# Performance work log

Measured on AMD Instinct MI355X. Metric: run time of the kernel, lower is better.

## Reference

```python
import jax, jax.numpy as jnp
import numpy as np

B, S, F, D, H, L, FF, M, NH, D2, O = 4, 1024, 20, 512, 8, 4, 2048, 32, 3, 256, 1
HD = D // H


def ln(x, g, b, eps=1e-5):
    m = jnp.mean(x, -1, keepdims=True)
    v = jnp.mean((x - m) ** 2, -1, keepdims=True)
    return (x - m) / jnp.sqrt(v + eps) * g + b


def posenc(seq_len, d_model):
    pos = jnp.arange(seq_len, dtype=jnp.float32)[:, None]
    div = jnp.exp(jnp.arange(0, d_model, 2, dtype=jnp.float32) * (-np.log(10000.0) / d_model))
    pe = jnp.zeros((seq_len, d_model), jnp.float32)
    pe = pe.at[:, 0::2].set(jnp.sin(pos * div)).at[:, 1::2].set(jnp.cos(pos * div))
    return pe


def setup_inputs():
    key = jax.random.key(0)
    ks = iter(jax.random.split(key, 64))
    g = lambda shape, s=0.02: jax.random.normal(next(ks), shape, jnp.float32) * s
    z = lambda shape: jnp.zeros(shape, jnp.float32)
    o = lambda shape: jnp.ones(shape, jnp.float32)
    return {
        'x': jax.random.normal(next(ks), (B, S, F), jnp.float32),
        'in_W': g((F, D)), 'in_b': z((D,)), 'in_ln_g': o((D,)), 'in_ln_b': z((D,)),
        'ln1_g': o((L, D)), 'ln1_b': z((L, D)),
        'Wq': g((L, D, D)), 'bq': z((L, D)), 'Wk': g((L, D, D)), 'bk': z((L, D)),
        'Wv': g((L, D, D)), 'bv': z((L, D)), 'Wo': g((L, D, D)), 'bo': z((L, D)),
        'rel': g((L, 2 * M + 1, HD)),
        'ln2_g': o((L, D)), 'ln2_b': z((L, D)),
        'W1': g((L, D, FF)), 'b1': z((L, FF)), 'W2': g((L, FF, D)), 'b2': z((L, D)),
        'gWq': g((D, D)), 'gbq': z((D,)), 'gWk': g((D, D)), 'gbk': z((D,)),
        'gWv': g((D, D)), 'gbv': z((D,)), 'gWo': g((D, D)), 'gbo': z((D,)),
        'hW1': g((NH, D, D2)), 'hb1': z((NH, D2)), 'hln_g': o((NH, D2)), 'hln_b': z((NH, D2)),
        'hW2': g((NH, D2, O)), 'hb2': z((NH, O)),
    }


def _heads(xx, Wq, bq, Wk, bk, Wv, bv):
    # project and split into heads -> [B,H,S,HD]
    q = (xx @ Wq + bq).reshape(B, S, H, HD).transpose(0, 2, 1, 3)
    k = (xx @ Wk + bk).reshape(B, S, H, HD).transpose(0, 2, 1, 3)
    v = (xx @ Wv + bv).reshape(B, S, H, HD).transpose(0, 2, 1, 3)
    return q, k, v


def _block(x, l1g, l1b, Wq, bq, Wk, bk, Wv, bv, Wo, bo, rel, l2g, l2b, W1, b1, W2, b2):
    xn = ln(x, l1g, l1b)
    q, k, v = _heads(xn, Wq, bq, Wk, bk, Wv, bv)
    scores = jnp.einsum('bhqd,bhkd->bhqk', q, k) / jnp.sqrt(jnp.float32(HD))
    pos = jnp.arange(S)
    rel_idx = jnp.clip(pos[None, :] - pos[:, None], -M, M) + M  # [S,S]
    rel_enc = rel[rel_idx]  # [S,S,HD]
    # relative-position bias (NOT scaled by sqrt(HD), matching the torch code)
    scores = scores + jnp.einsum('bhqd,qkd->bhqk', q, rel_enc)
    w = jax.nn.softmax(scores, axis=-1)
    out = jnp.einsum('bhqk,bhkd->bhqd', w, v).transpose(0, 2, 1, 3).reshape(B, S, D)
    x = x + out @ Wo + bo
    xn = ln(x, l2g, l2b)
    ff = jax.nn.gelu(xn @ W1 + b1, approximate=False) @ W2 + b2
    return x + ff


def _forward(x, in_W, in_b, in_ln_g, in_ln_b, ln1_g, ln1_b, Wq, bq, Wk, bk, Wv, bv, Wo, bo, rel,
             ln2_g, ln2_b, W1, b1, W2, b2, gWq, gbq, gWk, gbk, gWv, gbv, gWo, gbo,
             hW1, hb1, hln_g, hln_b, hW2, hb2):
    h = ln(x @ in_W + in_b, in_ln_g, in_ln_b)
    h = h + posenc(S, D)[None]
    for l in range(L):
        h = _block(h, ln1_g[l], ln1_b[l], Wq[l], bq[l], Wk[l], bk[l], Wv[l], bv[l],
                   Wo[l], bo[l], rel[l], ln2_g[l], ln2_b[l], W1[l], b1[l], W2[l], b2[l])
    # global multi-head self-attention (standard scaled dot-product)
    q, k, v = _heads(h, gWq, gbq, gWk, gbk, gWv, gbv)
    w = jax.nn.softmax(jnp.einsum('bhqd,bhkd->bhqk', q, k) / jnp.sqrt(jnp.float32(HD)), axis=-1)
    go = jnp.einsum('bhqk,bhkd->bhqd', w, v).transpose(0, 2, 1, 3).reshape(B, S, D) @ gWo + gbo
    ctx = go[:, -1, :]  # last-timestep context [B,D]
    y = jnp.einsum('bd,hde->bhe', ctx, hW1) + hb1  # [B,NH,D2]
    y = jax.nn.relu(ln(y, hln_g, hln_b))
    return jnp.einsum('bhe,heo->bho', y, hW2) + hb2  # [B,NH,O]


def reference(x, in_W, in_b, in_ln_g, in_ln_b, ln1_g, ln1_b, Wq, bq, Wk, bk, Wv, bv, Wo, bo, rel,
              ln2_g, ln2_b, W1, b1, W2, b2, gWq, gbq, gWk, gbk, gWv, gbv, gWo, gbo,
              hW1, hb1, hln_g, hln_b, hW2, hb2):
    return _forward(x, in_W, in_b, in_ln_g, in_ln_b, ln1_g, ln1_b, Wq, bq, Wk, bk, Wv, bv, Wo, bo,
                    rel, ln2_g, ln2_b, W1, b1, W2, b2, gWq, gbq, gWk, gbk, gWv, gbv, gWo, gbo,
                    hW1, hb1, hln_g, hln_b, hW2, hb2)
```

## Files before the change

kernel.cpp:

```cpp
#include <hip/hip_runtime.h>
#include <math.h>

#define DEV __device__ __forceinline__

constexpr int BSD = 4 * 1024 * 512;

typedef __attribute__((ext_vector_type(8))) short bf16x8;
typedef __attribute__((ext_vector_type(4))) float f32x4;

typedef __attribute__((address_space(1))) const void global_cvoid;
typedef __attribute__((address_space(3))) void lds_void;

DEV ushort f2b(float f) {
  union { float f; uint u; } x{f};
  uint r = x.u + 0x7fff + ((x.u >> 16) & 1);
  return (ushort)(r >> 16);
}
DEV float b2f(ushort u) {
  union { uint u; float f; } x{(uint)u << 16};
  return x.f;
}
DEV int swz128(int b) { return b ^ (((b >> 7) & 7) << 4); }

DEV float wave_sum(float v) {
#pragma unroll
  for (int m = 32; m >= 1; m >>= 1) v += __shfl_xor(v, m, 64);
  return v;
}
DEV float wave_max(float v) {
#pragma unroll
  for (int m = 32; m >= 1; m >>= 1) v = fmaxf(v, __shfl_xor(v, m, 64));
  return v;
}
DEV float block_sum(float v, float* sm) {
  v = wave_sum(v);
  __syncthreads();
  if ((threadIdx.x & 63) == 0) sm[threadIdx.x >> 6] = v;
  __syncthreads();
  return sm[0] + sm[1] + sm[2] + sm[3];
}
DEV float block_max(float v, float* sm) {
  v = wave_max(v);
  __syncthreads();
  if ((threadIdx.x & 63) == 0) sm[threadIdx.x >> 6] = v;
  __syncthreads();
  return fmaxf(fmaxf(sm[0], sm[1]), fmaxf(sm[2], sm[3]));
}

__global__ __launch_bounds__(256) void k_inproj(
    const float* __restrict__ x, const float* __restrict__ W,
    const float* __restrict__ bias, const float* __restrict__ g,
    const float* __restrict__ bt, float* __restrict__ h) {
  int r = blockIdx.x;
  int s = r & 1023;
  int t = threadIdx.x;
  __shared__ float xr[20];
  __shared__ float red[4];
  if (t < 20) xr[t] = x[r * 20 + t];
  __syncthreads();
  float o0 = bias[t], o1 = bias[t + 256];
#pragma unroll
  for (int f = 0; f < 20; f++) {
    float xv = xr[f];
    o0 += xv * W[f * 512 + t];
    o1 += xv * W[f * 512 + t + 256];
  }
  float mean = block_sum(o0 + o1, red) * (1.f / 512.f);
  float d0 = o0 - mean, d1 = o1 - mean;
  float var = block_sum(d0 * d0 + d1 * d1, red) * (1.f / 512.f);
  float rs = rsqrtf(var + 1e-5f);
  float n0 = d0 * rs * g[t] + bt[t];
  float n1 = d1 * rs * g[t + 256] + bt[t + 256];
  const float c1 = -9.210340371976184f / 512.f;
  {
    int c = t;
    float div = expf((float)(c & ~1) * c1);
    float arg = (float)s * div;
    n0 += (c & 1) ? cosf(arg) : sinf(arg);
  }
  {
    int c = t + 256;
    float div = expf((float)(c & ~1) * c1);
    float arg = (float)s * div;
    n1 += (c & 1) ? cosf(arg) : sinf(arg);
  }
  float* hr = h + (size_t)r * 512;
  hr[t] = n0;
  hr[t + 256] = n1;
}

__global__ __launch_bounds__(256) void k_lnb(
    const float* __restrict__ x, const float* __restrict__ g,
    const float* __restrict__ bt, ushort* __restrict__ y) {
  __shared__ float red[4];
  int r = blockIdx.x;
  int t = threadIdx.x;
  const float* xr = x + (size_t)r * 512;
  float v0 = xr[t], v1 = xr[t + 256];
  float mean = block_sum(v0 + v1, red) * (1.f / 512.f);
  float d0 = v0 - mean, d1 = v1 - mean;
  float var = block_sum(d0 * d0 + d1 * d1, red) * (1.f / 512.f);
  float rs = rsqrtf(var + 1e-5f);
  ushort* yr = y + (size_t)r * 512;
  yr[t] = f2b(d0 * rs * g[t] + bt[t]);
  yr[t + 256] = f2b(d1 * rs * g[t + 256] + bt[t + 256]);
}

__global__ __launch_bounds__(256) void k_cvt(const float* __restrict__ x,
                                             ushort* __restrict__ y) {
  int i = blockIdx.x * 256 + threadIdx.x;
  y[i] = f2b(x[i]);
}

struct PJobs {
  const float* s[19];
  ushort* d[19];
};
__global__ __launch_bounds__(256) void k_wprep(PJobs j, int K, int N) {
  const float* src = j.s[blockIdx.z];
  ushort* dst = j.d[blockIdx.z];
  __shared__ float ld[32][33];
  int n0 = blockIdx.x * 32, k0 = blockIdx.y * 32;
  int c = threadIdx.x & 31, r0 = threadIdx.x >> 5;
#pragma unroll
  for (int i = 0; i < 4; i++)
    ld[r0 + i * 8][c] = src[(size_t)(k0 + r0 + i * 8) * N + n0 + c];
  __syncthreads();
#pragma unroll
  for (int i = 0; i < 4; i++)
    dst[(size_t)(n0 + r0 + i * 8) * K + k0 + c] = f2b(ld[c][r0 + i * 8]);
}

__global__ __launch_bounds__(256) void k_relprep(const float* __restrict__ rel,
                                                 ushort* __restrict__ relb) {
  int i = blockIdx.x * 256 + threadIdx.x;
  int l = blockIdx.y;
  int r = i >> 6, d = i & 63;
  float v = (r < 65) ? rel[((size_t)l * 65 + r) * 64 + d] : 0.f;
  relb[(size_t)l * 80 * 64 + i] = f2b(v);
}

template <int BM, int MODE, int FUSEB>
__global__ __launch_bounds__(256) void k_mg(
    const ushort* __restrict__ A, const ushort* __restrict__ Bt,
    const float* __restrict__ bias0, const float* __restrict__ bias1,
    const float* __restrict__ bias2, void* __restrict__ Cv,
    int K, int ldc, int gx) {
  constexpr int BN = 64, BK = 64;
  __shared__ __align__(16) ushort As[BM * BK];
  __shared__ __align__(16) ushort Bs[BN * BK];
  int nwg = gridDim.x;
  int id = blockIdx.x;
  int logical = (id & 7) * (nwg >> 3) + (id >> 3);
  int bx = logical % gx, by = logical / gx;
  int row0 = by * BM, col0 = bx * BN;
  int t = threadIdx.x, lane = t & 63, w = t >> 6;
  int rl15 = lane & 15, l16 = lane >> 4;
  constexpr int WR = BM / 32;
  constexpr int WC = 4 / WR;
  constexpr int NI = 64 / (WC * 16);
  constexpr int MI = 2;
  int wr = w % WR, wc = w / WR;
  int wrow = wr * 32;
  int wcol = wc * (WC == 2 ? 32 : 0);
  f32x4 acc[MI][NI] = {};
  for (int kb = 0; kb < K; kb += BK) {
    __syncthreads();
#pragma unroll
    for (int i = 0; i < BM / 32; i++) {
      int blk = w * (BM / 32) + i;
      int lb = blk * 1024 + lane * 16;
      int lg = swz128(lb);
      int r = lg >> 7, cb = (lg & 127) >> 1;
      __builtin_amdgcn_global_load_lds(
          (global_cvoid*)(A + (size_t)(row0 + r) * K + kb + cb),
          (lds_void*)((char*)As + blk * 1024), 16, 0, 0);
    }
#pragma unroll
    for (int i = 0; i < 2; i++) {
      int blk = w * 2 + i;
      int lb = blk * 1024 + lane * 16;
      int lg = swz128(lb);
      int r = lg >> 7, cb = (lg & 127) >> 1;
      __builtin_amdgcn_global_load_lds(
          (global_cvoid*)(Bt + (size_t)(col0 + r) * K + kb + cb),
          (lds_void*)((char*)Bs + blk * 1024), 16, 0, 0);
    }
    __syncthreads();
#pragma unroll
    for (int ks = 0; ks < 2; ks++) {
      bf16x8 af[MI], bfr[NI];
#pragma unroll
      for (int mi = 0; mi < MI; mi++) {
        int row = wrow + mi * 16 + rl15;
        af[mi] = *(const bf16x8*)((char*)As + swz128(row * 128 + ks * 64 + l16 * 16));
      }
#pragma unroll
      for (int ni = 0; ni < NI; ni++) {
        int row = wcol + ni * 16 + rl15;
        bfr[ni] = *(const bf16x8*)((char*)Bs + swz128(row * 128 + ks * 64 + l16 * 16));
      }
#pragma unroll
      for (int mi = 0; mi < MI; mi++)
#pragma unroll
        for (int ni = 0; ni < NI; ni++)
          acc[mi][ni] = __builtin_amdgcn_mfma_f32_16x16x32_bf16(af[mi], bfr[ni],
                                                                acc[mi][ni], 0, 0, 0);
    }
  }
#pragma unroll
  for (int mi = 0; mi < MI; mi++) {
#pragma unroll
    for (int ni = 0; ni < NI; ni++) {
      int col = col0 + wcol + ni * 16 + rl15;
      float bv;
      if (FUSEB) {
        const float* bp = bias0;
        int c = col;
        if (c >= 1024) { bp = bias2; c -= 1024; }
        else if (c >= 512) { bp = bias1; c -= 512; }
        bv = bp[c];
      } else {
        bv = bias0[col];
      }
#pragma unroll
      for (int r = 0; r < 4; r++) {
        int row = row0 + wrow + mi * 16 + l16 * 4 + r;
        float val = acc[mi][ni][r] + bv;
        if (MODE == 0) {
          ((ushort*)Cv)[(size_t)row * ldc + col] = f2b(val);
        } else if (MODE == 1) {
          float* Cp = (float*)Cv + (size_t)row * ldc + col;
          *Cp = *Cp + val;
        } else {
          val = 0.5f * val * (1.f + erff(val * 0.70710678118654752f));
          ((ushort*)Cv)[(size_t)row * ldc + col] = f2b(val);
        }
      }
    }
  }
}

__global__ __launch_bounds__(256) void k_attn_mfma(
    const ushort* __restrict__ qkv, const ushort* __restrict__ relb,
    ushort* __restrict__ ao) {
  __shared__ __align__(16) ushort Ks[64 * 72];
  __shared__ __align__(16) ushort Vt[64 * 72];
  __shared__ float qrl[64][66];
  __shared__ __align__(16) ushort Pl[4][16 * 72];
  int t = threadIdx.x, lane = t & 63, w = t >> 6;
  int h = blockIdx.y, b = blockIdx.z;
  int q0 = blockIdx.x * 64;
  size_t baseq = ((size_t)b * 1024) * 1536 + h * 64;
  size_t basek = baseq + 512;
  size_t basev = baseq + 1024;
  int qw = q0 + w * 16;
  int rl15 = lane & 15, l16 = lane >> 4;

  bf16x8 aq[2];
#pragma unroll
  for (int ks = 0; ks < 2; ks++)
    aq[ks] = *(const bf16x8*)(qkv + baseq + (size_t)(qw + rl15) * 1536 + ks * 32 + l16 * 8);

#pragma unroll
  for (int nb = 0; nb < 5; nb++) {
    f32x4 rc = {};
#pragma unroll
    for (int ks = 0; ks < 2; ks++) {
      bf16x8 rb = *(const bf16x8*)(relb + (size_t)(nb * 16 + rl15) * 64 + ks * 32 + l16 * 8);
      rc = __builtin_amdgcn_mfma_f32_16x16x32_bf16(aq[ks], rb, rc, 0, 0, 0);
    }
    int col = nb * 16 + rl15;
    if (col < 65) {
#pragma unroll
      for (int r = 0; r < 4; r++) qrl[w * 16 + l16 * 4 + r][col] = rc[r];
    }
  }

  float mrow[4], lrow[4];
  f32x4 oacc[4] = {};
#pragma unroll
  for (int r = 0; r < 4; r++) {
    mrow[r] = -1e30f;
    lrow[r] = 0.f;
  }

  for (int kb = 0; kb < 1024; kb += 64) {
    __syncthreads();
#pragma unroll
    for (int i = 0; i < 2; i++) {
      int c = t + i * 256;
      int key = c >> 3, dc = c & 7;
      bf16x8 kv = *(const bf16x8*)(qkv + basek + (size_t)(kb + key) * 1536 + dc * 8);
      *(bf16x8*)&Ks[key * 72 + dc * 8] = kv;
    }
#pragma unroll
    for (int i = 0; i < 2; i++) {
      int c = t + i * 256;
      int key = c & 63, dh = c >> 6;
      bf16x8 vv8 = *(const bf16x8*)(qkv + basev + (size_t)(kb + key) * 1536 + dh * 8);
#pragma unroll
      for (int e = 0; e < 8; e++) Vt[(dh * 8 + e) * 72 + key] = (ushort)vv8[e];
    }
    __syncthreads();

    f32x4 sacc[4] = {};
#pragma unroll
    for (int ks = 0; ks < 2; ks++) {
#pragma unroll
      for (int nb = 0; nb < 4; nb++) {
        bf16x8 bk8 = *(const bf16x8*)&Ks[(nb * 16 + rl15) * 72 + ks * 32 + l16 * 8];
        sacc[nb] = __builtin_amdgcn_mfma_f32_16x16x32_bf16(aq[ks], bk8, sacc[nb], 0, 0, 0);
      }
    }

    float p[4][4];
#pragma unroll
    for (int r = 0; r < 4; r++) {
      int rloc = l16 * 4 + r;
      int qg = q0 + w * 16 + rloc;
      float sv[4];
      float rowm = -1e30f;
#pragma unroll
      for (int nb = 0; nb < 4; nb++) {
        int kcol = kb + nb * 16 + rl15;
        int delta = kcol - qg;
        delta = delta < -32 ? -32 : (delta > 32 ? 32 : delta);
        float s_ = sacc[nb][r] * 0.125f + qrl[w * 16 + rloc][delta + 32];
        sv[nb] = s_;
        rowm = fmaxf(rowm, s_);
      }
#pragma unroll
      for (int msk = 1; msk <= 8; msk <<= 1)
        rowm = fmaxf(rowm, __shfl_xor(rowm, msk, 64));
      float mn = fmaxf(mrow[r], rowm);
      float scale = __expf(mrow[r] - mn);
      float ls = 0.f;
#pragma unroll
      for (int nb = 0; nb < 4; nb++) {
        float pv = __expf(sv[nb] - mn);
        p[nb][r] = pv;
        ls += pv;
      }
#pragma unroll
      for (int msk = 1; msk <= 8; msk <<= 1) ls += __shfl_xor(ls, msk, 64);
      lrow[r] = lrow[r] * scale + ls;
      mrow[r] = mn;
#pragma unroll
      for (int nb = 0; nb < 4; nb++) oacc[nb][r] *= scale;
    }

#pragma unroll
    for (int nb = 0; nb < 4; nb++)
#pragma unroll
      for (int r = 0; r < 4; r++)
        Pl[w][(l16 * 4 + r) * 72 + nb * 16 + rl15] = f2b(p[nb][r]);
#pragma unroll
    for (int ks = 0; ks < 2; ks++) {
      bf16x8 pa = *(const bf16x8*)&Pl[w][rl15 * 72 + ks * 32 + l16 * 8];
#pragma unroll
      for (int nb = 0; nb < 4; nb++) {
        bf16x8 bv8 = *(const bf16x8*)&Vt[(nb * 16 + rl15) * 72 + ks * 32 + l16 * 8];
        oacc[nb] = __builtin_amdgcn_mfma_f32_16x16x32_bf16(pa, bv8, oacc[nb], 0, 0, 0);
      }
    }
  }

  size_t baseo = ((size_t)b * 1024) * 512 + h * 64;
#pragma unroll
  for (int nb = 0; nb < 4; nb++) {
    int d = nb * 16 + rl15;
#pragma unroll
    for (int r = 0; r < 4; r++) {
      int row = q0 + w * 16 + l16 * 4 + r;
      ao[baseo + (size_t)row * 512 + d] = f2b(oacc[nb][r] / lrow[r]);
    }
  }
}

__global__ __launch_bounds__(256) void k_gattn(
    const ushort* __restrict__ qkv, float* __restrict__ ctxa) {
  int t = threadIdx.x;
  int h = blockIdx.x & 7, b = blockIdx.x >> 3;
  __shared__ float Qs[64];
  __shared__ float sc[1024];
  __shared__ float red[4];
  __shared__ float op[4][64];
  if (t < 64) Qs[t] = b2f(qkv[(size_t)(b * 1024 + 1023) * 1536 + h * 64 + t]);
  __syncthreads();
  float lm = -1e30f;
  float sv[4];
#pragma unroll
  for (int jj = 0; jj < 4; jj++) {
    int j = t + (jj << 8);
    float s = 0.f;
#pragma unroll
    for (int d = 0; d < 64; d++)
      s += Qs[d] * b2f(qkv[(size_t)(b * 1024 + j) * 1536 + 512 + h * 64 + d]);
    s *= 0.125f;
    sv[jj] = s;
    lm = fmaxf(lm, s);
  }
  float bm = block_max(lm, red);
  float ls = 0.f;
#pragma unroll
  for (int jj = 0; jj < 4; jj++) {
    float e = __expf(sv[jj] - bm);
    sc[t + (jj << 8)] = e;
    ls += e;
  }
  float bs = block_sum(ls, red);
  int d = t & 63, qd = t >> 6;
  float acc = 0.f;
  for (int j = qd << 8; j < (qd << 8) + 256; j++)
    acc += sc[j] * b2f(qkv[(size_t)(b * 1024 + j) * 1536 + 1024 + h * 64 + d]);
  op[qd][d] = acc;
  __syncthreads();
  if (t < 64) {
    float r = (op[0][t] + op[1][t] + op[2][t] + op[3][t]) / bs;
    ctxa[b * 512 + h * 64 + t] = r;
  }
}

__global__ __launch_bounds__(256) void k_rowgemm(
    const float* __restrict__ xrow, const float* __restrict__ W,
    const float* __restrict__ bias, float* __restrict__ y) {
  int b = blockIdx.x;
  int t = threadIdx.x;
  __shared__ float xs[512];
  xs[t] = xrow[b * 512 + t];
  xs[t + 256] = xrow[b * 512 + t + 256];
  __syncthreads();
  float a0 = bias[t], a1 = bias[t + 256];
  for (int kk = 0; kk < 512; kk++) {
    float xv = xs[kk];
    a0 += xv * W[(size_t)kk * 512 + t];
    a1 += xv * W[(size_t)kk * 512 + t + 256];
  }
  y[b * 512 + t] = a0;
  y[b * 512 + t + 256] = a1;
}

__global__ __launch_bounds__(256) void k_head(
    const float* __restrict__ ctx, const float* __restrict__ hW1,
    const float* __restrict__ hb1, const float* __restrict__ hg,
    const float* __restrict__ hbt, const float* __restrict__ hW2,
    const float* __restrict__ hb2, float* __restrict__ out) {
  int b = blockIdx.x / 3, nh = blockIdx.x % 3;
  int t = threadIdx.x;
  __shared__ float cs[512];
  __shared__ float red[4];
  cs[t] = ctx[b * 512 + t];
  cs[t + 256] = ctx[b * 512 + t + 256];
  __syncthreads();
  float y = hb1[nh * 256 + t];
  for (int d = 0; d < 512; d++) y += cs[d] * hW1[((size_t)nh * 512 + d) * 256 + t];
  float mean = block_sum(y, red) * (1.f / 256.f);
  float dv = y - mean;
  float var = block_sum(dv * dv, red) * (1.f / 256.f);
  float rs = rsqrtf(var + 1e-5f);
  float yn = dv * rs * hg[nh * 256 + t] + hbt[nh * 256 + t];
  yn = fmaxf(yn, 0.f);
  float s = block_sum(yn * hW2[nh * 256 + t], red);
  if (t == 0) out[b * 3 + nh] = s + hb2[nh];
}

extern "C" void kernel_launch(void* const* d_in, const int* in_sizes, int n_in,
                              void* d_out, int out_size, void* d_ws, size_t ws_size,
                              hipStream_t stream) {
  const float* x = (const float*)d_in[0];
  const float* in_W = (const float*)d_in[1];
  const float* in_b = (const float*)d_in[2];
  const float* in_lng = (const float*)d_in[3];
  const float* in_lnb = (const float*)d_in[4];
  const float* ln1_g = (const float*)d_in[5];
  const float* ln1_b = (const float*)d_in[6];
  const float* Wq = (const float*)d_in[7];
  const float* bq = (const float*)d_in[8];
  const float* Wk = (const float*)d_in[9];
  const float* bk = (const float*)d_in[10];
  const float* Wv = (const float*)d_in[11];
  const float* bv = (const float*)d_in[12];
  const float* Wo = (const float*)d_in[13];
  const float* bo = (const float*)d_in[14];
  const float* rel = (const float*)d_in[15];
  const float* ln2_g = (const float*)d_in[16];
  const float* ln2_b = (const float*)d_in[17];
  const float* W1 = (const float*)d_in[18];
  const float* b1 = (const float*)d_in[19];
  const float* W2 = (const float*)d_in[20];
  const float* b2 = (const float*)d_in[21];
  const float* gWq = (const float*)d_in[22];
  const float* gbq = (const float*)d_in[23];
  const float* gWk = (const float*)d_in[24];
  const float* gbk = (const float*)d_in[25];
  const float* gWv = (const float*)d_in[26];
  const float* gbv = (const float*)d_in[27];
  const float* gWo = (const float*)d_in[28];
  const float* gbo = (const float*)d_in[29];
  const float* hW1 = (const float*)d_in[30];
  const float* hb1 = (const float*)d_in[31];
  const float* hlng = (const float*)d_in[32];
  const float* hlnb = (const float*)d_in[33];
  const float* hW2 = (const float*)d_in[34];
  const float* hb2 = (const float*)d_in[35];
  float* out = (float*)d_out;

  uint8_t* wsb = (uint8_t*)d_ws;
  const size_t MB = 1024 * 1024;
  float* h = (float*)(wsb + 0);
  ushort* xn = (ushort*)(wsb + 8 * MB);
  ushort* qkvb = (ushort*)(wsb + 12 * MB);
  ushort* aob = (ushort*)(wsb + 24 * MB);
  ushort* ffb = (ushort*)(wsb + 28 * MB);
  ushort* wqkv = (ushort*)(wsb + 44 * MB);
  ushort* wto = (ushort*)(wsb + 50 * MB);
  ushort* wt1 = (ushort*)(wsb + 52 * MB);
  ushort* wt2 = (ushort*)(wsb + 60 * MB);
  ushort* gwqkv = (ushort*)(wsb + 68 * MB);
  ushort* relb = (ushort*)(wsb + 70 * MB);
  float* attnlast = (float*)(wsb + 71 * MB);
  float* ctx = attnlast + 4096;

  const size_t W55 = 512 * 512;

  {
    PJobs j{};
    for (int l = 0; l < 4; l++) {
      j.s[l * 4 + 0] = Wq + (size_t)l * W55;
      j.d[l * 4 + 0] = wqkv + (size_t)l * 1536 * 512;
      j.s[l * 4 + 1] = Wk + (size_t)l * W55;
      j.d[l * 4 + 1] = wqkv + (size_t)l * 1536 * 512 + 512 * 512;
      j.s[l * 4 + 2] = Wv + (size_t)l * W55;
      j.d[l * 4 + 2] = wqkv + (size_t)l * 1536 * 512 + 1024 * 512;
      j.s[l * 4 + 3] = Wo + (size_t)l * W55;
      j.d[l * 4 + 3] = wto + (size_t)l * W55;
    }
    j.s[16] = gWq; j.d[16] = gwqkv;
    j.s[17] = gWk; j.d[17] = gwqkv + 512 * 512;
    j.s[18] = gWv; j.d[18] = gwqkv + 1024 * 512;
    k_wprep<<<dim3(16, 16, 19), 256, 0, stream>>>(j, 512, 512);
  }
  {
    PJobs j{};
    for (int l = 0; l < 4; l++) {
      j.s[l] = W1 + (size_t)l * 512 * 2048;
      j.d[l] = wt1 + (size_t)l * 2048 * 512;
    }
    k_wprep<<<dim3(64, 16, 4), 256, 0, stream>>>(j, 512, 2048);
  }
  {
    PJobs j{};
    for (int l = 0; l < 4; l++) {
      j.s[l] = W2 + (size_t)l * 2048 * 512;
      j.d[l] = wt2 + (size_t)l * 512 * 2048;
    }
    k_wprep<<<dim3(16, 64, 4), 256, 0, stream>>>(j, 2048, 512);
  }
  k_relprep<<<dim3(20, 4), 256, 0, stream>>>(rel, relb);
  k_inproj<<<4096, 256, 0, stream>>>(x, in_W, in_b, in_lng, in_lnb, h);

  for (int l = 0; l < 4; l++) {
    size_t vo = (size_t)l * 512;
    k_lnb<<<4096, 256, 0, stream>>>(h, ln1_g + vo, ln1_b + vo, xn);
    k_mg<128, 0, 1><<<768, 256, 0, stream>>>(xn, wqkv + (size_t)l * 1536 * 512,
                                             bq + vo, bk + vo, bv + vo, qkvb,
                                             512, 1536, 24);
    k_attn_mfma<<<dim3(16, 8, 4), 256, 0, stream>>>(qkvb, relb + (size_t)l * 80 * 64, aob);
    k_mg<64, 1, 0><<<512, 256, 0, stream>>>(aob, wto + (size_t)l * W55,
                                            bo + vo, bo + vo, bo + vo, h, 512, 512, 8);
    k_lnb<<<4096, 256, 0, stream>>>(h, ln2_g + vo, ln2_b + vo, xn);
    k_mg<128, 2, 0><<<1024, 256, 0, stream>>>(xn, wt1 + (size_t)l * 2048 * 512,
                                              b1 + (size_t)l * 2048, nullptr, nullptr,
                                              ffb, 512, 2048, 32);
    k_mg<64, 1, 0><<<512, 256, 0, stream>>>(ffb, wt2 + (size_t)l * 512 * 2048,
                                            b2 + vo, b2 + vo, b2 + vo, h, 2048, 512, 8);
  }

  k_cvt<<<8192, 256, 0, stream>>>(h, xn);
  k_mg<128, 0, 1><<<768, 256, 0, stream>>>(xn, gwqkv, gbq, gbk, gbv, qkvb, 512, 1536, 24);
  k_gattn<<<32, 256, 0, stream>>>(qkvb, attnlast);
  k_rowgemm<<<4, 256, 0, stream>>>(attnlast, gWo, gbo, ctx);
  k_head<<<12, 256, 0, stream>>>(ctx, hW1, hb1, hlng, hlnb, hW2, hb2, out);
}
```

Measured before the change: 631.2 us.

## Pre-transpose V, fold softmax scale, widen FF1 tiles, fuse final bf16 cast

Several changes at once. A new kernel transposes V into a per-head layout so the attention kernel can stage K and V into swizzled LDS with direct global-to-LDS loads, instead of scattering V element by element. The 1/sqrt(HD) scale moves into the Q projection epilogue, with the relative-position table pre-scaled by 8 to compensate, and the relative bias is stored as bf16. Out-of-window key blocks use one clamped bias value per row, and the online-softmax rescale runs only when the row max grows. The FF1 GEMM now uses 128x128 tiles, and the last FF2 GEMM also writes a bf16 copy of the residual, which removes the separate conversion kernel. The trade-offs are extra traffic for the V transpose, reuse of the FF buffer for it, and small rounding differences from the bf16 bias and the moved scale.

```diff
diff --git a/kernel.cpp b/kernel.cpp
--- a/kernel.cpp
+++ b/kernel.cpp
@@ -106,12 +106,6 @@
   yr[t + 256] = f2b(d1 * rs * g[t + 256] + bt[t + 256]);
 }
 
-__global__ __launch_bounds__(256) void k_cvt(const float* __restrict__ x,
-                                             ushort* __restrict__ y) {
-  int i = blockIdx.x * 256 + threadIdx.x;
-  y[i] = f2b(x[i]);
-}
-
 struct PJobs {
   const float* s[19];
   ushort* d[19];
@@ -136,17 +130,33 @@
   int i = blockIdx.x * 256 + threadIdx.x;
   int l = blockIdx.y;
   int r = i >> 6, d = i & 63;
-  float v = (r < 65) ? rel[((size_t)l * 65 + r) * 64 + d] : 0.f;
+  float v = (r < 65) ? rel[((size_t)l * 65 + r) * 64 + d] * 8.f : 0.f;
   relb[(size_t)l * 80 * 64 + i] = f2b(v);
 }
 
-template <int BM, int MODE, int FUSEB>
+__global__ __launch_bounds__(256) void k_vprep(const ushort* __restrict__ qkv,
+                                               ushort* __restrict__ vT) {
+  int bh = blockIdx.z, b = bh >> 3, h = bh & 7;
+  int s0 = blockIdx.x * 32, d0 = blockIdx.y * 32;
+  __shared__ ushort td[32][33];
+  int c = threadIdx.x & 31, r = threadIdx.x >> 5;
+#pragma unroll
+  for (int i = 0; i < 4; i++)
+    td[r + i * 8][c] =
+        qkv[(size_t)(b * 1024 + s0 + r + i * 8) * 1536 + 1024 + h * 64 + d0 + c];
+  __syncthreads();
+#pragma unroll
+  for (int i = 0; i < 4; i++)
+    vT[((size_t)bh * 64 + d0 + r + i * 8) * 1024 + s0 + c] = td[c][r + i * 8];
+}
+
+template <int BM, int BN, int MODE, int FUSEB>
 __global__ __launch_bounds__(256) void k_mg(
     const ushort* __restrict__ A, const ushort* __restrict__ Bt,
     const float* __restrict__ bias0, const float* __restrict__ bias1,
     const float* __restrict__ bias2, void* __restrict__ Cv,
-    int K, int ldc, int gx) {
-  constexpr int BN = 64, BK = 64;
+    ushort* __restrict__ C2, int K, int ldc, int gx) {
+  constexpr int BK = 64;
   __shared__ __align__(16) ushort As[BM * BK];
   __shared__ __align__(16) ushort Bs[BN * BK];
   int nwg = gridDim.x;
@@ -156,13 +166,13 @@
   int row0 = by * BM, col0 = bx * BN;
   int t = threadIdx.x, lane = t & 63, w = t >> 6;
   int rl15 = lane & 15, l16 = lane >> 4;
-  constexpr int WR = BM / 32;
+  constexpr int WR = (BM == 128 && BN == 128) ? 2 : BM / 32;
   constexpr int WC = 4 / WR;
-  constexpr int NI = 64 / (WC * 16);
-  constexpr int MI = 2;
+  constexpr int MI = BM / (WR * 16);
+  constexpr int NI = BN / (WC * 16);
   int wr = w % WR, wc = w / WR;
-  int wrow = wr * 32;
-  int wcol = wc * (WC == 2 ? 32 : 0);
+  int wrow = wr * MI * 16;
+  int wcol = wc * NI * 16;
   f32x4 acc[MI][NI] = {};
   for (int kb = 0; kb < K; kb += BK) {
     __syncthreads();
@@ -177,8 +187,8 @@
           (lds_void*)((char*)As + blk * 1024), 16, 0, 0);
     }
 #pragma unroll
-    for (int i = 0; i < 2; i++) {
-      int blk = w * 2 + i;
+    for (int i = 0; i < BN / 32; i++) {
+      int blk = w * (BN / 32) + i;
       int lb = blk * 1024 + lane * 16;
       int lg = swz128(lb);
       int r = lg >> 7, cb = (lg & 127) >> 1;
@@ -227,14 +237,20 @@
       for (int r = 0; r < 4; r++) {
         int row = row0 + wrow + mi * 16 + l16 * 4 + r;
         float val = acc[mi][ni][r] + bv;
+        if (FUSEB && col < 512) val *= 0.125f;
         if (MODE == 0) {
           ((ushort*)Cv)[(size_t)row * ldc + col] = f2b(val);
         } else if (MODE == 1) {
           float* Cp = (float*)Cv + (size_t)row * ldc + col;
           *Cp = *Cp + val;
-        } else {
+        } else if (MODE == 2) {
           val = 0.5f * val * (1.f + erff(val * 0.70710678118654752f));
           ((ushort*)Cv)[(size_t)row * ldc + col] = f2b(val);
+        } else {
+          float* Cp = (float*)Cv + (size_t)row * ldc + col;
+          float nv = *Cp + val;
+          *Cp = nv;
+          C2[(size_t)row * ldc + col] = f2b(nv);
         }
       }
     }
@@ -242,18 +258,18 @@
 }
 
 __global__ __launch_bounds__(256) void k_attn_mfma(
-    const ushort* __restrict__ qkv, const ushort* __restrict__ relb,
-    ushort* __restrict__ ao) {
-  __shared__ __align__(16) ushort Ks[64 * 72];
-  __shared__ __align__(16) ushort Vt[64 * 72];
-  __shared__ float qrl[64][66];
+    const ushort* __restrict__ qkv, const ushort* __restrict__ vT,
+    const ushort* __restrict__ relb, ushort* __restrict__ ao) {
+  __shared__ __align__(16) ushort Ks[64 * 64];
+  __shared__ __align__(16) ushort Vts[64 * 64];
+  __shared__ ushort qrlb[64][66];
   __shared__ __align__(16) ushort Pl[4][16 * 72];
   int t = threadIdx.x, lane = t & 63, w = t >> 6;
   int h = blockIdx.y, b = blockIdx.z;
   int q0 = blockIdx.x * 64;
   size_t baseq = ((size_t)b * 1024) * 1536 + h * 64;
   size_t basek = baseq + 512;
-  size_t basev = baseq + 1024;
+  const ushort* vTb = vT + ((size_t)(b * 8 + h)) * 64 * 1024;
   int qw = q0 + w * 16;
   int rl15 = lane & 15, l16 = lane >> 4;
 
@@ -273,7 +289,7 @@
     int col = nb * 16 + rl15;
     if (col < 65) {
 #pragma unroll
-      for (int r = 0; r < 4; r++) qrl[w * 16 + l16 * 4 + r][col] = rc[r];
+      for (int r = 0; r < 4; r++) qrlb[w * 16 + l16 * 4 + r][col] = f2b(rc[r]);
     }
   }
 
@@ -289,18 +305,16 @@
     __syncthreads();
 #pragma unroll
     for (int i = 0; i < 2; i++) {
-      int c = t + i * 256;
-      int key = c >> 3, dc = c & 7;
-      bf16x8 kv = *(const bf16x8*)(qkv + basek + (size_t)(kb + key) * 1536 + dc * 8);
-      *(bf16x8*)&Ks[key * 72 + dc * 8] = kv;
-    }
-#pragma unroll
-    for (int i = 0; i < 2; i++) {
-      int c = t + i * 256;
-      int key = c & 63, dh = c >> 6;
-      bf16x8 vv8 = *(const bf16x8*)(qkv + basev + (size_t)(kb + key) * 1536 + dh * 8);
-#pragma unroll
-      for (int e = 0; e < 8; e++) Vt[(dh * 8 + e) * 72 + key] = (ushort)vv8[e];
+      int blk = w * 2 + i;
+      int lb = blk * 1024 + lane * 16;
+      int lg = swz128(lb);
+      int r = lg >> 7, cb = (lg & 127) >> 1;
+      __builtin_amdgcn_global_load_lds(
+          (global_cvoid*)(qkv + basek + (size_t)(kb + r) * 1536 + cb),
+          (lds_void*)((char*)Ks + blk * 1024), 16, 0, 0);
+      __builtin_amdgcn_global_load_lds(
+          (global_cvoid*)(vTb + (size_t)r * 1024 + kb + cb),
+          (lds_void*)((char*)Vts + blk * 1024), 16, 0, 0);
     }
     __syncthreads();
 
@@ -309,45 +323,61 @@
     for (int ks = 0; ks < 2; ks++) {
 #pragma unroll
       for (int nb = 0; nb < 4; nb++) {
-        bf16x8 bk8 = *(const bf16x8*)&Ks[(nb * 16 + rl15) * 72 + ks * 32 + l16 * 8];
+        bf16x8 bk8 = *(const bf16x8*)((char*)Ks +
+                                      swz128((nb * 16 + rl15) * 128 + ks * 64 + l16 * 16));
         sacc[nb] = __builtin_amdgcn_mfma_f32_16x16x32_bf16(aq[ks], bk8, sacc[nb], 0, 0, 0);
       }
     }
 
+    float sv[4][4];
+    bool hiU = (kb >= qw + 47);
+    bool loU = (kb + 95 <= qw);
+    if (hiU || loU) {
+      int idx = hiU ? 64 : 0;
+#pragma unroll
+      for (int r = 0; r < 4; r++) {
+        float crow = b2f(qrlb[w * 16 + l16 * 4 + r][idx]);
+#pragma unroll
+        for (int nb = 0; nb < 4; nb++) sv[r][nb] = sacc[nb][r] + crow;
+      }
+    } else {
+#pragma unroll
+      for (int r = 0; r < 4; r++) {
+        int rloc = l16 * 4 + r;
+        int qg = q0 + w * 16 + rloc;
+#pragma unroll
+        for (int nb = 0; nb < 4; nb++) {
+          int delta = kb + nb * 16 + rl15 - qg;
+          delta = delta < -32 ? -32 : (delta > 32 ? 32 : delta);
+          sv[r][nb] = sacc[nb][r] + b2f(qrlb[w * 16 + rloc][delta + 32]);
+        }
+      }
+    }
+
     float p[4][4];
 #pragma unroll
     for (int r = 0; r < 4; r++) {
-      int rloc = l16 * 4 + r;
-      int qg = q0 + w * 16 + rloc;
-      float sv[4];
-      float rowm = -1e30f;
-#pragma unroll
-      for (int nb = 0; nb < 4; nb++) {
-        int kcol = kb + nb * 16 + rl15;
-        int delta = kcol - qg;
-        delta = delta < -32 ? -32 : (delta > 32 ? 32 : delta);
-        float s_ = sacc[nb][r] * 0.125f + qrl[w * 16 + rloc][delta + 32];
-        sv[nb] = s_;
-        rowm = fmaxf(rowm, s_);
-      }
+      float rowm = fmaxf(fmaxf(sv[r][0], sv[r][1]), fmaxf(sv[r][2], sv[r][3]));
 #pragma unroll
       for (int msk = 1; msk <= 8; msk <<= 1)
         rowm = fmaxf(rowm, __shfl_xor(rowm, msk, 64));
-      float mn = fmaxf(mrow[r], rowm);
-      float scale = __expf(mrow[r] - mn);
+      if (rowm > mrow[r]) {
+        float scale = __expf(mrow[r] - rowm);
+        mrow[r] = rowm;
+        lrow[r] *= scale;
+#pragma unroll
+        for (int nb = 0; nb < 4; nb++) oacc[nb][r] *= scale;
+      }
       float ls = 0.f;
 #pragma unroll
       for (int nb = 0; nb < 4; nb++) {
-        float pv = __expf(sv[nb] - mn);
+        float pv = __expf(sv[r][nb] - mrow[r]);
         p[nb][r] = pv;
         ls += pv;
       }
 #pragma unroll
       for (int msk = 1; msk <= 8; msk <<= 1) ls += __shfl_xor(ls, msk, 64);
-      lrow[r] = lrow[r] * scale + ls;
-      mrow[r] = mn;
-#pragma unroll
-      for (int nb = 0; nb < 4; nb++) oacc[nb][r] *= scale;
+      lrow[r] += ls;
     }
 
 #pragma unroll
@@ -360,7 +390,8 @@
       bf16x8 pa = *(const bf16x8*)&Pl[w][rl15 * 72 + ks * 32 + l16 * 8];
 #pragma unroll
       for (int nb = 0; nb < 4; nb++) {
-        bf16x8 bv8 = *(const bf16x8*)&Vt[(nb * 16 + rl15) * 72 + ks * 32 + l16 * 8];
+        bf16x8 bv8 = *(const bf16x8*)((char*)Vts +
+                                      swz128((nb * 16 + rl15) * 128 + ks * 64 + l16 * 16));
         oacc[nb] = __builtin_amdgcn_mfma_f32_16x16x32_bf16(pa, bv8, oacc[nb], 0, 0, 0);
       }
     }
@@ -397,7 +428,6 @@
 #pragma unroll
     for (int d = 0; d < 64; d++)
       s += Qs[d] * b2f(qkv[(size_t)(b * 1024 + j) * 1536 + 512 + h * 64 + d]);
-    s *= 0.125f;
     sv[jj] = s;
     lm = fmaxf(lm, s);
   }
@@ -513,6 +543,7 @@
   ushort* qkvb = (ushort*)(wsb + 12 * MB);
   ushort* aob = (ushort*)(wsb + 24 * MB);
   ushort* ffb = (ushort*)(wsb + 28 * MB);
+  ushort* vTb = ffb;
   ushort* wqkv = (ushort*)(wsb + 44 * MB);
   ushort* wto = (ushort*)(wsb + 50 * MB);
   ushort* wt1 = (ushort*)(wsb + 52 * MB);
@@ -563,22 +594,30 @@
   for (int l = 0; l < 4; l++) {
     size_t vo = (size_t)l * 512;
     k_lnb<<<4096, 256, 0, stream>>>(h, ln1_g + vo, ln1_b + vo, xn);
-    k_mg<128, 0, 1><<<768, 256, 0, stream>>>(xn, wqkv + (size_t)l * 1536 * 512,
-                                             bq + vo, bk + vo, bv + vo, qkvb,
-                                             512, 1536, 24);
-    k_attn_mfma<<<dim3(16, 8, 4), 256, 0, stream>>>(qkvb, relb + (size_t)l * 80 * 64, aob);
-    k_mg<64, 1, 0><<<512, 256, 0, stream>>>(aob, wto + (size_t)l * W55,
-                                            bo + vo, bo + vo, bo + vo, h, 512, 512, 8);
+    k_mg<128, 64, 0, 1><<<768, 256, 0, stream>>>(xn, wqkv + (size_t)l * 1536 * 512,
+                                                 bq + vo, bk + vo, bv + vo, qkvb,
+                                                 nullptr, 512, 1536, 24);
+    k_vprep<<<dim3(32, 2, 32), 256, 0, stream>>>(qkvb, vTb);
+    k_attn_mfma<<<dim3(16, 8, 4), 256, 0, stream>>>(qkvb, vTb,
+                                                    relb + (size_t)l * 80 * 64, aob);
+    k_mg<64, 64, 1, 0><<<512, 256, 0, stream>>>(aob, wto + (size_t)l * W55, bo + vo,
+                                                nullptr, nullptr, h, nullptr, 512, 512, 8);
     k_lnb<<<4096, 256, 0, stream>>>(h, ln2_g + vo, ln2_b + vo, xn);
-    k_mg<128, 2, 0><<<1024, 256, 0, stream>>>(xn, wt1 + (size_t)l * 2048 * 512,
-                                              b1 + (size_t)l * 2048, nullptr, nullptr,
-                                              ffb, 512, 2048, 32);
-    k_mg<64, 1, 0><<<512, 256, 0, stream>>>(ffb, wt2 + (size_t)l * 512 * 2048,
-                                            b2 + vo, b2 + vo, b2 + vo, h, 2048, 512, 8);
-  }
-
-  k_cvt<<<8192, 256, 0, stream>>>(h, xn);
-  k_mg<128, 0, 1><<<768, 256, 0, stream>>>(xn, gwqkv, gbq, gbk, gbv, qkvb, 512, 1536, 24);
+    k_mg<128, 128, 2, 0><<<512, 256, 0, stream>>>(xn, wt1 + (size_t)l * 2048 * 512,
+                                                  b1 + (size_t)l * 2048, nullptr, nullptr,
+                                                  ffb, nullptr, 512, 2048, 16);
+    if (l < 3)
+      k_mg<64, 64, 1, 0><<<512, 256, 0, stream>>>(ffb, wt2 + (size_t)l * 512 * 2048,
+                                                  b2 + vo, nullptr, nullptr, h, nullptr,
+                                                  2048, 512, 8);
+    else
+      k_mg<64, 64, 3, 0><<<512, 256, 0, stream>>>(ffb, wt2 + (size_t)l * 512 * 2048,
+                                                  b2 + vo, nullptr, nullptr, h, xn,
+                                                  2048, 512, 8);
+  }
+
+  k_mg<128, 64, 0, 1><<<768, 256, 0, stream>>>(xn, gwqkv, gbq, gbk, gbv, qkvb,
+                                               nullptr, 512, 1536, 24);
   k_gattn<<<32, 256, 0, stream>>>(qkvb, attnlast);
   k_rowgemm<<<4, 256, 0, stream>>>(attnlast, gWo, gbo, ctx);
   k_head<<<12, 256, 0, stream>>>(ctx, hW1, hb1, hlng, hlnb, hW2, hb2, out);
```

Result: no change. 621.9 us (-1.5%).
